# Kernel optimization log

Measured on AMD Instinct MI355X. Metric: run time of the kernel, lower is better.

Reference implementation:

```python
import jax, jax.numpy as jnp
import numpy as np

B, D, H, W, C = 1, 16, 56, 56, 128
NH = 4
WD, WH, WW = 8, 7, 7          # window size (t, h, w)
SD, SH, SW = 4, 3, 3          # shift size
N = WD * WH * WW              # tokens per window = 392
HEAD = C // NH
SCALE = HEAD ** -0.5
HID = 4 * C                   # mlp_ratio = 4
REL_TAB = (2 * WD - 1) * (2 * WH - 1) * (2 * WW - 1)


def _rel_pos_index():
    coords = np.stack(np.meshgrid(np.arange(WD), np.arange(WH), np.arange(WW), indexing='ij'))
    cf = coords.reshape(3, -1)
    rel = (cf[:, :, None] - cf[:, None, :]).transpose(1, 2, 0).astype(np.int64)
    rel[..., 0] += WD - 1; rel[..., 1] += WH - 1; rel[..., 2] += WW - 1
    rel[..., 0] *= (2 * WH - 1) * (2 * WW - 1)
    rel[..., 1] *= (2 * WW - 1)
    return rel.sum(-1)  # (N, N)

REL_IDX = jnp.asarray(_rel_pos_index())


def _win_part_np(x):
    b, d, h, w, c = x.shape
    x = x.reshape(b, d // WD, WD, h // WH, WH, w // WW, WW, c)
    return x.transpose(0, 1, 3, 5, 2, 4, 6, 7).reshape(-1, N, c)


def _attn_mask():
    # shifted-window mask, computed once on host (static)
    img = np.zeros((1, D, H, W, 1))
    cnt = 0
    for ds in (slice(0, -WD), slice(-WD, -SD), slice(-SD, None)):
        for hs in (slice(0, -WH), slice(-WH, -SH), slice(-SH, None)):
            for ws in (slice(0, -WW), slice(-WW, -SW), slice(-SW, None)):
                img[:, ds, hs, ws, :] = cnt
                cnt += 1
    mw = _win_part_np(img).reshape(-1, N)
    am = mw[:, None, :] - mw[:, :, None]
    return np.where(am != 0, -100.0, 0.0).astype(np.float32)  # (nW, N, N)

ATTN_MASK = jnp.asarray(_attn_mask())


def layer_norm(x, w, b, eps=1e-5):
    mu = x.mean(-1, keepdims=True)
    var = ((x - mu) ** 2).mean(-1, keepdims=True)
    return (x - mu) * jax.lax.rsqrt(var + eps) * w + b


def window_partition(x):
    b = x.shape[0]
    x = x.reshape(b, D // WD, WD, H // WH, WH, W // WW, WW, C)
    return x.transpose(0, 1, 3, 5, 2, 4, 6, 7).reshape(-1, N, C)


def window_reverse(win, b):
    x = win.reshape(b, D // WD, H // WH, W // WW, WD, WH, WW, C)
    return x.transpose(0, 1, 4, 2, 5, 3, 6, 7).reshape(b, D, H, W, C)


def setup_inputs() -> dict:
    key = jax.random.key(0)
    ks = jax.random.split(key, 16)
    s = 0.02
    return {
        'x': jax.random.normal(ks[0], (B, D, H, W, C), jnp.float32),
        'norm1_w': jnp.ones((C,), jnp.float32),
        'norm1_b': jnp.zeros((C,), jnp.float32),
        'qkv_w': jax.random.normal(ks[1], (3 * C, C), jnp.float32) * s,
        'qkv_b': jnp.zeros((3 * C,), jnp.float32),
        'rel_pos_table': jax.random.normal(ks[2], (REL_TAB, NH), jnp.float32) * s,
        'proj_w': jax.random.normal(ks[3], (C, C), jnp.float32) * s,
        'proj_b': jnp.zeros((C,), jnp.float32),
        'norm2_w': jnp.ones((C,), jnp.float32),
        'norm2_b': jnp.zeros((C,), jnp.float32),
        'fc1_w': jax.random.normal(ks[4], (HID, C), jnp.float32) * s,
        'fc1_b': jnp.zeros((HID,), jnp.float32),
        'fc2_w': jax.random.normal(ks[5], (C, HID), jnp.float32) * s,
        'fc2_b': jnp.zeros((C,), jnp.float32),
    }


def reference(x, norm1_w, norm1_b, qkv_w, qkv_b, rel_pos_table, proj_w, proj_b,
              norm2_w, norm2_b, fc1_w, fc1_b, fc2_w, fc2_b):
    shortcut = x
    h = layer_norm(x, norm1_w, norm1_b)
    # cyclic shift
    h = jnp.roll(h, shift=(-SD, -SH, -SW), axis=(1, 2, 3))
    win = window_partition(h)                      # (B*nW, N, C)
    Bw = win.shape[0]
    qkv = win @ qkv_w.T + qkv_b                    # (Bw, N, 3C)
    qkv = qkv.reshape(Bw, N, 3, NH, HEAD).transpose(2, 0, 3, 1, 4)
    q, k, v = qkv[0] * SCALE, qkv[1], qkv[2]       # (Bw, NH, N, HEAD)
    bias = rel_pos_table[REL_IDX].transpose(2, 0, 1)  # (NH, N, N)
    A = jnp.einsum('bhnc,bhmc->bhnm', q, k) + bias[None]
    nW = Bw // B
    A = A.reshape(B, nW, NH, N, N) + ATTN_MASK[None, :, None]
    A = jax.nn.softmax(A.reshape(Bw, NH, N, N), axis=-1)
    y = jnp.einsum('bhnm,bhmc->bhnc', A, v).transpose(0, 2, 1, 3).reshape(Bw, N, C)
    y = y @ proj_w.T + proj_b
    h = window_reverse(y, B)
    h = jnp.roll(h, shift=(SD, SH, SW), axis=(1, 2, 3))
    x = shortcut + h
    # Mlp module: internal LayerNorm + residual (see Mlp.forward_fn)
    m = layer_norm(x, norm2_w, norm2_b)
    m = jax.nn.gelu(m @ fc1_w.T + fc1_b, approximate=False)
    m = m @ fc2_w.T + fc2_b
    return x + m
```

## Files before the change

### kernel.cpp

```cpp
#include <hip/hip_runtime.h>
#include <hip/hip_bf16.h>
#include <math.h>


typedef short s16x8 __attribute__((ext_vector_type(8)));
typedef unsigned short u16x8 __attribute__((ext_vector_type(8)));
typedef float fp32x4 __attribute__((ext_vector_type(4)));

#define T_TOT 50176
#define N_TOK 392
#define N_WIN 128

__device__ __forceinline__ unsigned short f2bf(float f) {
    union { float f; unsigned u; } v; v.f = f;
    unsigned r = v.u + 0x7FFFu + ((v.u >> 16) & 1u);
    return (unsigned short)(r >> 16);
}
__device__ __forceinline__ float bf2f(unsigned short u) {
    union { unsigned u; float f; } v; v.u = ((unsigned)u) << 16;
    return v.f;
}

__global__ void cvt_w_k(const float* __restrict__ wq, const float* __restrict__ wp,
                        const float* __restrict__ w1, const float* __restrict__ w2,
                        unsigned short* __restrict__ oq, unsigned short* __restrict__ op,
                        unsigned short* __restrict__ o1, unsigned short* __restrict__ o2)
{
    int i = blockIdx.x * 256 + threadIdx.x;
    if (i < 384 * 128) oq[i] = f2bf(wq[i]);
    if (i < 128 * 128) op[i] = f2bf(wp[i]);
    if (i < 512 * 128) { o1[i] = f2bf(w1[i]); o2[i] = f2bf(w2[i]); }
}

__global__ void bias_tab_k(const float* __restrict__ tab, float* __restrict__ out)
{
    int idx = blockIdx.x * 256 + threadIdx.x;
    if (idx >= 4 * N_TOK * N_TOK) return;
    int h = idx / (N_TOK * N_TOK), r = idx % (N_TOK * N_TOK);
    int i = r / N_TOK, j = r % N_TOK;
    int di = i / 49, hi = (i % 49) / 7, wi = i % 7;
    int dj = j / 49, hj = (j % 49) / 7, wj = j % 7;
    int rel = (di - dj + 7) * 169 + (hi - hj + 6) * 13 + (wi - wj + 6);
    out[idx] = tab[rel * 4 + h];
}

__global__ __launch_bounds__(256) void ln1_part_k(
    const float* __restrict__ x, const float* __restrict__ w,
    const float* __restrict__ b, unsigned short* __restrict__ xw)
{
    const int t = blockIdx.x * 4 + (threadIdx.x >> 6);
    const int lane = threadIdx.x & 63;
    const int win = t / N_TOK, n = t % N_TOK;
    const int wd = win >> 6, wh = (win >> 3) & 7, ww = win & 7;
    const int td = n / 49, rr = n % 49, th = rr / 7, tw = rr % 7;
    const int gd = wd * 8 + td, gh = wh * 7 + th, gw = ww * 7 + tw;
    const int sd = (gd + 4) & 15;
    int sh = gh + 3; if (sh >= 56) sh -= 56;
    int sw = gw + 3; if (sw >= 56) sw -= 56;
    const float* px = x + (((size_t)sd * 56 + sh) * 56 + sw) * 128;
    float v0 = px[lane], v1 = px[lane + 64];
    float s = v0 + v1, s2 = v0 * v0 + v1 * v1;
#pragma unroll
    for (int o = 32; o > 0; o >>= 1) { s += __shfl_xor(s, o); s2 += __shfl_xor(s2, o); }
    float mu = s * (1.f / 128.f);
    float var = s2 * (1.f / 128.f) - mu * mu;
    float rstd = rsqrtf(var + 1e-5f);
    unsigned short* po = xw + (size_t)t * 128;
    po[lane]      = f2bf((v0 - mu) * rstd * w[lane]      + b[lane]);
    po[lane + 64] = f2bf((v1 - mu) * rstd * w[lane + 64] + b[lane + 64]);
}

__global__ __launch_bounds__(256) void ln2_k(
    const float* __restrict__ x1, const float* __restrict__ w,
    const float* __restrict__ b, unsigned short* __restrict__ xn)
{
    const int t = blockIdx.x * 4 + (threadIdx.x >> 6);
    const int lane = threadIdx.x & 63;
    const float* px = x1 + (size_t)t * 128;
    float v0 = px[lane], v1 = px[lane + 64];
    float s = v0 + v1, s2 = v0 * v0 + v1 * v1;
#pragma unroll
    for (int o = 32; o > 0; o >>= 1) { s += __shfl_xor(s, o); s2 += __shfl_xor(s2, o); }
    float mu = s * (1.f / 128.f);
    float var = s2 * (1.f / 128.f) - mu * mu;
    float rstd = rsqrtf(var + 1e-5f);
    unsigned short* po = xn + (size_t)t * 128;
    po[lane]      = f2bf((v0 - mu) * rstd * w[lane]      + b[lane]);
    po[lane + 64] = f2bf((v1 - mu) * rstd * w[lane + 64] + b[lane + 64]);
}

template<int K, int EPI>
__global__ __launch_bounds__(256, 2) void gemm_k(
    const unsigned short* __restrict__ A,
    const unsigned short* __restrict__ Bt,
    const float* __restrict__ bias,
    const float* __restrict__ resid,
    void* __restrict__ outp)
{
    __shared__ __align__(16) unsigned short Asl[128 * 64];
    __shared__ __align__(16) unsigned short Bsl[128 * 64];
    const int bm = blockIdx.x * 128;
    const int bn = blockIdx.y * 128;
    const int tid = threadIdx.x;
    const int lane = tid & 63;
    const int wave = tid >> 6;
    const int wr = wave >> 1, wc = wave & 1;
    const int lr = lane & 15;
    const int lk = (lane >> 4) << 3;

    fp32x4 acc[4][4];
#pragma unroll
    for (int i = 0; i < 4; ++i)
#pragma unroll
        for (int j = 0; j < 4; ++j) acc[i][j] = {0.f, 0.f, 0.f, 0.f};

    for (int ks = 0; ks < K; ks += 64) {
        __syncthreads();
#pragma unroll
        for (int it = 0; it < 4; ++it) {
            int chunk = it * 256 + tid;
            int row = chunk >> 3;
            int kc = (chunk & 7) << 3;
            *(uint4*)&Asl[row * 64 + kc] =
                *(const uint4*)&A[(size_t)(bm + row) * K + ks + kc];
            *(uint4*)&Bsl[row * 64 + kc] =
                *(const uint4*)&Bt[(size_t)(bn + row) * K + ks + kc];
        }
        __syncthreads();
#pragma unroll
        for (int kk = 0; kk < 64; kk += 32) {
            s16x8 af[4], bfr[4];
#pragma unroll
            for (int mb = 0; mb < 4; ++mb)
                af[mb] = *(const s16x8*)&Asl[(wr * 64 + mb * 16 + lr) * 64 + kk + lk];
#pragma unroll
            for (int nb = 0; nb < 4; ++nb)
                bfr[nb] = *(const s16x8*)&Bsl[(wc * 64 + nb * 16 + lr) * 64 + kk + lk];
#pragma unroll
            for (int mb = 0; mb < 4; ++mb)
#pragma unroll
                for (int nb = 0; nb < 4; ++nb)
                    acc[mb][nb] = __builtin_amdgcn_mfma_f32_16x16x32_bf16(
                        af[mb], bfr[nb], acc[mb][nb], 0, 0, 0);
        }
    }

    const int crow = (lane >> 4) << 2;
    const int ccol = lane & 15;
#pragma unroll
    for (int mb = 0; mb < 4; ++mb) {
#pragma unroll
        for (int nb = 0; nb < 4; ++nb) {
#pragma unroll
            for (int r = 0; r < 4; ++r) {
                const int grow = bm + wr * 64 + mb * 16 + crow + r;
                const int gcol = bn + wc * 64 + nb * 16 + ccol;
                float v = acc[mb][nb][r] + bias[gcol];
                if (EPI == 0) {
                    if (gcol < 128) v *= 0.17677669529663687f;
                    ((unsigned short*)outp)[(size_t)grow * 384 + gcol] = f2bf(v);
                } else if (EPI == 1) {
                    int w  = grow / N_TOK, n = grow % N_TOK;
                    int wd = w >> 6, wh = (w >> 3) & 7, ww = w & 7;
                    int td = n / 49, rr = n % 49, th = rr / 7, tw = rr % 7;
                    int gd = wd * 8 + td, gh = wh * 7 + th, gw = ww * 7 + tw;
                    int sd = (gd + 4) & 15;
                    int sh = gh + 3; if (sh >= 56) sh -= 56;
                    int sw = gw + 3; if (sw >= 56) sw -= 56;
                    size_t oi = (((size_t)sd * 56 + sh) * 56 + sw) * 128 + gcol;
                    ((float*)outp)[oi] = v + resid[oi];
                } else if (EPI == 2) {
                    v = 0.5f * v * (1.f + erff(v * 0.70710678118654752f));
                    ((unsigned short*)outp)[(size_t)grow * 512 + gcol] = f2bf(v);
                } else {
                    size_t oi = (size_t)grow * 128 + gcol;
                    ((float*)outp)[oi] = v + resid[oi];
                }
            }
        }
    }
}

#define KSTR 40
#define VSTR 424
#define PTS  40

__global__ __launch_bounds__(256, 2) void attn_k(
    const unsigned short* __restrict__ qkv,
    const float* __restrict__ btab,
    unsigned short* __restrict__ y)
{
    __shared__ __align__(16) unsigned short Ksh[416 * KSTR];
    __shared__ __align__(16) unsigned short Vt[32 * VSTR];
    __shared__ __align__(16) unsigned short Pt[4][16 * PTS];
    __shared__ __align__(4) unsigned char rid_sh[416];

    const int blk = blockIdx.x;
    const int wI = blk >> 2, h = blk & 3;
    const int tid = threadIdx.x;
    const int wave = tid >> 6, lane = tid & 63;
    const int lr = lane & 15, g = lane >> 4, lk = g << 3;
    const unsigned short* base = qkv + (size_t)wI * N_TOK * 384;

    const int wd = wI >> 6, wh = (wI >> 3) & 7, ww = wI & 7;
    const bool boundary = (wd == 1) | (wh == 7) | (ww == 7);

    for (int idx = tid; idx < 392 * 4; idx += 256) {
        int j = idx >> 2, c0 = (idx & 3) << 3;
        *(uint4*)&Ksh[j * KSTR + c0] =
            *(const uint4*)&base[(size_t)j * 384 + 128 + h * 32 + c0];
    }
    for (int idx = tid; idx < 24 * 4; idx += 256) {
        int j = 392 + (idx >> 2), c0 = (idx & 3) << 3;
        u16x8 z = {};
        *(u16x8*)&Ksh[j * KSTR + c0] = z;
    }
    for (int idx = tid; idx < 32 * 49; idx += 256) {
        int c = idx & 31, j0 = (idx >> 5) << 3;
        const unsigned short* vp = base + 256 + h * 32 + c;
        u16x8 tmp;
#pragma unroll
        for (int i = 0; i < 8; ++i) tmp[i] = vp[(size_t)(j0 + i) * 384];
        *(u16x8*)&Vt[c * VSTR + j0] = tmp;
    }
    for (int idx = tid; idx < 32 * 3; idx += 256) {
        int c = idx & 31, j0 = 392 + ((idx >> 5) << 3);
        u16x8 z = {};
        *(u16x8*)&Vt[c * VSTR + j0] = z;
    }
    for (int n = tid; n < 416; n += 256) {
        int nn = (n < 392) ? n : 391;
        int td = nn / 49, rr = nn % 49, th = rr / 7, tw = rr % 7;
        int gd = wd * 8 + td, gh = wh * 7 + th, gw = ww * 7 + tw;
        int r = ((gd < 8) ? 0 : ((gd < 12) ? 9 : 18)) +
                ((gh < 49) ? 0 : ((gh < 53) ? 3 : 6)) +
                ((gw < 49) ? 0 : ((gw < 53) ? 1 : 2));
        rid_sh[n] = (unsigned char)r;
    }
    __syncthreads();

    const float* bb = btab + (size_t)h * N_TOK * N_TOK;
    unsigned short* pw = &Pt[wave][0];
    const int j0 = g << 2;

    for (int rt = wave; rt < 25; rt += 4) {
        const int irow = rt * 16 + lr;
        const int ic = (irow < 392) ? irow : 391;
        s16x8 bq = *(const s16x8*)&base[(size_t)ic * 384 + h * 32 + lk];
        fp32x4 acc[25];
#pragma unroll
        for (int ct = 0; ct < 25; ++ct) {
            s16x8 ak = *(const s16x8*)&Ksh[(ct * 16 + lr) * KSTR + lk];
            fp32x4 z = {0.f, 0.f, 0.f, 0.f};
            acc[ct] = __builtin_amdgcn_mfma_f32_16x16x32_bf16(ak, bq, z, 0, 0, 0);
        }
        const int ri = rid_sh[ic];
        float mx = -1e30f;
#pragma unroll
        for (int ct = 0; ct < 24; ++ct) {
            float4 bv = *(const float4*)&bb[(size_t)ic * N_TOK + ct * 16 + j0];
            unsigned rj4 = *(const unsigned*)&rid_sh[ct * 16 + j0];
            const float bs[4] = {bv.x, bv.y, bv.z, bv.w};
#pragma unroll
            for (int r = 0; r < 4; ++r) {
                float s = acc[ct][r] + bs[r];
                int rj = (rj4 >> (8 * r)) & 255;
                if (boundary && rj != ri) s -= 100.f;
                acc[ct][r] = s;
                mx = fmaxf(mx, s);
            }
        }
        {
            float4 bv = {0.f, 0.f, 0.f, 0.f};
            unsigned rj4 = 0;
            if (g < 2) {
                bv = *(const float4*)&bb[(size_t)ic * N_TOK + 384 + j0];
                rj4 = *(const unsigned*)&rid_sh[384 + j0];
            }
            const float bs[4] = {bv.x, bv.y, bv.z, bv.w};
#pragma unroll
            for (int r = 0; r < 4; ++r) {
                float s = -1e30f;
                if (g < 2) {
                    s = acc[24][r] + bs[r];
                    int rj = (rj4 >> (8 * r)) & 255;
                    if (boundary && rj != ri) s -= 100.f;
                }
                acc[24][r] = s;
                mx = fmaxf(mx, s);
            }
        }
        mx = fmaxf(mx, __shfl_xor(mx, 16));
        mx = fmaxf(mx, __shfl_xor(mx, 32));
        float sum = 0.f;
#pragma unroll
        for (int ct = 0; ct < 25; ++ct)
#pragma unroll
            for (int r = 0; r < 4; ++r) {
                float p = __expf(acc[ct][r] - mx);
                acc[ct][r] = p;
                sum += p;
            }
        sum += __shfl_xor(sum, 16);
        sum += __shfl_xor(sum, 32);
        const float rs = 1.f / sum;
        fp32x4 o0 = {0.f, 0.f, 0.f, 0.f}, o1 = {0.f, 0.f, 0.f, 0.f};
#pragma unroll
        for (int ks = 0; ks < 13; ++ks) {
            unsigned w0, w1, w2 = 0, w3 = 0;
            asm("v_cvt_pk_bf16_f32 %0, %1, %2"
                : "=v"(w0) : "v"(acc[2 * ks][0]), "v"(acc[2 * ks][1]));
            asm("v_cvt_pk_bf16_f32 %0, %1, %2"
                : "=v"(w1) : "v"(acc[2 * ks][2]), "v"(acc[2 * ks][3]));
            if (ks < 12) {
                asm("v_cvt_pk_bf16_f32 %0, %1, %2"
                    : "=v"(w2) : "v"(acc[2 * ks + 1][0]), "v"(acc[2 * ks + 1][1]));
                asm("v_cvt_pk_bf16_f32 %0, %1, %2"
                    : "=v"(w3) : "v"(acc[2 * ks + 1][2]), "v"(acc[2 * ks + 1][3]));
            }
            *(unsigned*)&pw[lr * PTS + j0]          = w0;
            *(unsigned*)&pw[lr * PTS + j0 + 2]      = w1;
            *(unsigned*)&pw[lr * PTS + 16 + j0]     = w2;
            *(unsigned*)&pw[lr * PTS + 16 + j0 + 2] = w3;
            s16x8 ap  = *(const s16x8*)&pw[lr * PTS + lk];
            s16x8 bv0 = *(const s16x8*)&Vt[lr * VSTR + ks * 32 + lk];
            s16x8 bv1 = *(const s16x8*)&Vt[(16 + lr) * VSTR + ks * 32 + lk];
            o0 = __builtin_amdgcn_mfma_f32_16x16x32_bf16(ap, bv0, o0, 0, 0, 0);
            o1 = __builtin_amdgcn_mfma_f32_16x16x32_bf16(ap, bv1, o1, 0, 0, 0);
        }
#pragma unroll
        for (int r = 0; r < 4; ++r) {
            const float rsr = __shfl(rs, (g << 2) + r);
            const int row = rt * 16 + (g << 2) + r;
            if (row < 392) {
                size_t ob = ((size_t)wI * N_TOK + row) * 128 + h * 32;
                y[ob + lr]      = f2bf(o0[r] * rsr);
                y[ob + 16 + lr] = f2bf(o1[r] * rsr);
            }
        }
    }
}

extern "C" void kernel_launch(void* const* d_in, const int* in_sizes, int n_in,
                              void* d_out, int out_size, void* d_ws, size_t ws_size,
                              hipStream_t stream)
{
    const float* x      = (const float*)d_in[0];
    const float* n1w    = (const float*)d_in[1];
    const float* n1b    = (const float*)d_in[2];
    const float* qkv_w  = (const float*)d_in[3];
    const float* qkv_b  = (const float*)d_in[4];
    const float* rpt    = (const float*)d_in[5];
    const float* proj_w = (const float*)d_in[6];
    const float* proj_b = (const float*)d_in[7];
    const float* n2w    = (const float*)d_in[8];
    const float* n2b    = (const float*)d_in[9];
    const float* fc1_w  = (const float*)d_in[10];
    const float* fc1_b  = (const float*)d_in[11];
    const float* fc2_w  = (const float*)d_in[12];
    const float* fc2_b  = (const float*)d_in[13];

    char* ws = (char*)d_ws;
    unsigned short* xw  = (unsigned short*)(ws);
    unsigned short* qkv = (unsigned short*)(ws + 12845056);
    unsigned short* y   = (unsigned short*)(ws + 51380224);
    float*          x1  = (float*)         (ws + 64225280);
    unsigned short* xn  = (unsigned short*)(ws + 89915392);
    unsigned short* hid = (unsigned short*)(ws + 102760448);
    unsigned short* wq  = (unsigned short*)(ws + 154140672);
    unsigned short* wp  = (unsigned short*)(ws + 154238976);
    unsigned short* w1  = (unsigned short*)(ws + 154271744);
    unsigned short* w2  = (unsigned short*)(ws + 154402816);
    float*          bt  = (float*)         (ws + 154533888);

    hipLaunchKernelGGL(cvt_w_k, dim3(256), dim3(256), 0, stream,
                       qkv_w, proj_w, fc1_w, fc2_w, wq, wp, w1, w2);
    hipLaunchKernelGGL(bias_tab_k, dim3((4 * N_TOK * N_TOK + 255) / 256), dim3(256),
                       0, stream, rpt, bt);
    hipLaunchKernelGGL(ln1_part_k, dim3(T_TOT / 4), dim3(256), 0, stream,
                       x, n1w, n1b, xw);
    hipLaunchKernelGGL((gemm_k<128, 0>), dim3(392, 3), dim3(256), 0, stream,
                       xw, wq, qkv_b, (const float*)nullptr, (void*)qkv);
    hipLaunchKernelGGL(attn_k, dim3(512), dim3(256), 0, stream, qkv, bt, y);
    hipLaunchKernelGGL((gemm_k<128, 1>), dim3(392, 1), dim3(256), 0, stream,
                       y, wp, proj_b, x, (void*)x1);
    hipLaunchKernelGGL(ln2_k, dim3(T_TOT / 4), dim3(256), 0, stream,
                       x1, n2w, n2b, xn);
    hipLaunchKernelGGL((gemm_k<128, 2>), dim3(392, 4), dim3(256), 0, stream,
                       xn, w1, fc1_b, (const float*)nullptr, (void*)hid);
    hipLaunchKernelGGL((gemm_k<512, 3>), dim3(392, 1), dim3(256), 0, stream,
                       hid, w2, fc2_b, x1, d_out);
}
```

Measured before the change: 257.2 us.

## Fuse LayerNorm2 into proj GEMM epilogue and precombine shift mask with bias

The proj GEMM epilogue now stages its tile in shared memory, adds the residual, and computes LayerNorm2 row by row. It writes both x1 and the normalized bf16 input for fc1, which removes the separate ln2 kernel and its re-read of x1. The relative-position bias table is also expanded into 8 mask variants per head with the -100 shift mask already applied, so the attention kernel does a plain float4 add instead of building region IDs and comparing them. The cost is a bias-table build eight times larger each call, which aliases into the hid buffer, and a larger shared-memory footprint in the EPI==1 GEMM.

```diff
diff --git a/kernel.cpp b/kernel.cpp
--- a/kernel.cpp
+++ b/kernel.cpp
@@ -10,6 +10,7 @@
 #define T_TOT 50176
 #define N_TOK 392
 #define N_WIN 128
+#define NN2 153664
 
 __device__ __forceinline__ unsigned short f2bf(float f) {
     union { float f; unsigned u; } v; v.f = f;
@@ -35,13 +36,22 @@
 __global__ void bias_tab_k(const float* __restrict__ tab, float* __restrict__ out)
 {
     int idx = blockIdx.x * 256 + threadIdx.x;
-    if (idx >= 4 * N_TOK * N_TOK) return;
-    int h = idx / (N_TOK * N_TOK), r = idx % (N_TOK * N_TOK);
+    if (idx >= 32 * NN2) return;
+    int ht = idx / NN2, r = idx % NN2;
+    int h = ht >> 3, type = ht & 7;
     int i = r / N_TOK, j = r % N_TOK;
     int di = i / 49, hi = (i % 49) / 7, wi = i % 7;
     int dj = j / 49, hj = (j % 49) / 7, wj = j % 7;
     int rel = (di - dj + 7) * 169 + (hi - hj + 6) * 13 + (wi - wj + 6);
-    out[idx] = tab[rel * 4 + h];
+    float v = tab[rel * 4 + h];
+    int ri = ((type & 4) ? (di < 4 ? 9 : 18) : 0) +
+             ((type & 2) ? (hi < 4 ? 3 : 6) : 0) +
+             ((type & 1) ? (wi < 4 ? 1 : 2) : 0);
+    int rj = ((type & 4) ? (dj < 4 ? 9 : 18) : 0) +
+             ((type & 2) ? (hj < 4 ? 3 : 6) : 0) +
+             ((type & 1) ? (wj < 4 ? 1 : 2) : 0);
+    if (ri != rj) v -= 100.f;
+    out[idx] = v;
 }
 
 __global__ __launch_bounds__(256) void ln1_part_k(
@@ -70,35 +80,21 @@
     po[lane + 64] = f2bf((v1 - mu) * rstd * w[lane + 64] + b[lane + 64]);
 }
 
-__global__ __launch_bounds__(256) void ln2_k(
-    const float* __restrict__ x1, const float* __restrict__ w,
-    const float* __restrict__ b, unsigned short* __restrict__ xn)
-{
-    const int t = blockIdx.x * 4 + (threadIdx.x >> 6);
-    const int lane = threadIdx.x & 63;
-    const float* px = x1 + (size_t)t * 128;
-    float v0 = px[lane], v1 = px[lane + 64];
-    float s = v0 + v1, s2 = v0 * v0 + v1 * v1;
-#pragma unroll
-    for (int o = 32; o > 0; o >>= 1) { s += __shfl_xor(s, o); s2 += __shfl_xor(s2, o); }
-    float mu = s * (1.f / 128.f);
-    float var = s2 * (1.f / 128.f) - mu * mu;
-    float rstd = rsqrtf(var + 1e-5f);
-    unsigned short* po = xn + (size_t)t * 128;
-    po[lane]      = f2bf((v0 - mu) * rstd * w[lane]      + b[lane]);
-    po[lane + 64] = f2bf((v1 - mu) * rstd * w[lane + 64] + b[lane + 64]);
-}
-
 template<int K, int EPI>
 __global__ __launch_bounds__(256, 2) void gemm_k(
     const unsigned short* __restrict__ A,
     const unsigned short* __restrict__ Bt,
     const float* __restrict__ bias,
     const float* __restrict__ resid,
-    void* __restrict__ outp)
-{
-    __shared__ __align__(16) unsigned short Asl[128 * 64];
-    __shared__ __align__(16) unsigned short Bsl[128 * 64];
+    const float* __restrict__ lnw,
+    const float* __restrict__ lnb,
+    void* __restrict__ outp,
+    void* __restrict__ outp2)
+{
+    constexpr int SMB = (EPI == 1) ? (128 * 132 * 4) : (2 * 128 * 64 * 2);
+    __shared__ __align__(16) char smem[SMB];
+    unsigned short* Asl = (unsigned short*)smem;
+    unsigned short* Bsl = Asl + 128 * 64;
     const int bm = blockIdx.x * 128;
     const int bn = blockIdx.y * 128;
     const int tid = threadIdx.x;
@@ -147,6 +143,51 @@
 
     const int crow = (lane >> 4) << 2;
     const int ccol = lane & 15;
+
+    if (EPI == 1) {
+        float* xs = (float*)smem;
+        __syncthreads();
+#pragma unroll
+        for (int mb = 0; mb < 4; ++mb)
+#pragma unroll
+            for (int nb = 0; nb < 4; ++nb)
+#pragma unroll
+                for (int r = 0; r < 4; ++r) {
+                    int row = wr * 64 + mb * 16 + crow + r;
+                    int col = wc * 64 + nb * 16 + ccol;
+                    xs[row * 132 + col] = acc[mb][nb][r] + bias[col];
+                }
+        __syncthreads();
+        const float wA = lnw[lane], wB = lnw[lane + 64];
+        const float bA = lnb[lane], bB = lnb[lane + 64];
+        float* x1o = (float*)outp;
+        unsigned short* xno = (unsigned short*)outp2;
+        for (int row = wave; row < 128; row += 4) {
+            const int grow = bm + row;
+            const int w = grow / N_TOK, n = grow % N_TOK;
+            const int wd = w >> 6, wh = (w >> 3) & 7, ww = w & 7;
+            const int td = n / 49, rr = n % 49, th = rr / 7, tw = rr % 7;
+            const int gd = wd * 8 + td, gh = wh * 7 + th, gw = ww * 7 + tw;
+            const int sd = (gd + 4) & 15;
+            int sh = gh + 3; if (sh >= 56) sh -= 56;
+            int sw = gw + 3; if (sw >= 56) sw -= 56;
+            const size_t tok = ((size_t)sd * 56 + sh) * 56 + sw;
+            float w0 = xs[row * 132 + lane]      + resid[tok * 128 + lane];
+            float w1 = xs[row * 132 + 64 + lane] + resid[tok * 128 + 64 + lane];
+            float s = w0 + w1, s2 = w0 * w0 + w1 * w1;
+#pragma unroll
+            for (int o = 32; o > 0; o >>= 1) { s += __shfl_xor(s, o); s2 += __shfl_xor(s2, o); }
+            float mu = s * (1.f / 128.f);
+            float var = s2 * (1.f / 128.f) - mu * mu;
+            float rstd = rsqrtf(var + 1e-5f);
+            x1o[tok * 128 + lane]      = w0;
+            x1o[tok * 128 + 64 + lane] = w1;
+            xno[tok * 128 + lane]      = f2bf((w0 - mu) * rstd * wA + bA);
+            xno[tok * 128 + 64 + lane] = f2bf((w1 - mu) * rstd * wB + bB);
+        }
+        return;
+    }
+
 #pragma unroll
     for (int mb = 0; mb < 4; ++mb) {
 #pragma unroll
@@ -159,16 +200,6 @@
                 if (EPI == 0) {
                     if (gcol < 128) v *= 0.17677669529663687f;
                     ((unsigned short*)outp)[(size_t)grow * 384 + gcol] = f2bf(v);
-                } else if (EPI == 1) {
-                    int w  = grow / N_TOK, n = grow % N_TOK;
-                    int wd = w >> 6, wh = (w >> 3) & 7, ww = w & 7;
-                    int td = n / 49, rr = n % 49, th = rr / 7, tw = rr % 7;
-                    int gd = wd * 8 + td, gh = wh * 7 + th, gw = ww * 7 + tw;
-                    int sd = (gd + 4) & 15;
-                    int sh = gh + 3; if (sh >= 56) sh -= 56;
-                    int sw = gw + 3; if (sw >= 56) sw -= 56;
-                    size_t oi = (((size_t)sd * 56 + sh) * 56 + sw) * 128 + gcol;
-                    ((float*)outp)[oi] = v + resid[oi];
                 } else if (EPI == 2) {
                     v = 0.5f * v * (1.f + erff(v * 0.70710678118654752f));
                     ((unsigned short*)outp)[(size_t)grow * 512 + gcol] = f2bf(v);
@@ -187,13 +218,12 @@
 
 __global__ __launch_bounds__(256, 2) void attn_k(
     const unsigned short* __restrict__ qkv,
-    const float* __restrict__ btab,
+    const float* __restrict__ cbias,
     unsigned short* __restrict__ y)
 {
     __shared__ __align__(16) unsigned short Ksh[416 * KSTR];
     __shared__ __align__(16) unsigned short Vt[32 * VSTR];
     __shared__ __align__(16) unsigned short Pt[4][16 * PTS];
-    __shared__ __align__(4) unsigned char rid_sh[416];
 
     const int blk = blockIdx.x;
     const int wI = blk >> 2, h = blk & 3;
@@ -203,7 +233,7 @@
     const unsigned short* base = qkv + (size_t)wI * N_TOK * 384;
 
     const int wd = wI >> 6, wh = (wI >> 3) & 7, ww = wI & 7;
-    const bool boundary = (wd == 1) | (wh == 7) | (ww == 7);
+    const int type = ((wd == 1) ? 4 : 0) | ((wh == 7) ? 2 : 0) | ((ww == 7) ? 1 : 0);
 
     for (int idx = tid; idx < 392 * 4; idx += 256) {
         int j = idx >> 2, c0 = (idx & 3) << 3;
@@ -216,30 +246,21 @@
         *(u16x8*)&Ksh[j * KSTR + c0] = z;
     }
     for (int idx = tid; idx < 32 * 49; idx += 256) {
-        int c = idx & 31, j0 = (idx >> 5) << 3;
+        int c = idx & 31, j0v = (idx >> 5) << 3;
         const unsigned short* vp = base + 256 + h * 32 + c;
         u16x8 tmp;
 #pragma unroll
-        for (int i = 0; i < 8; ++i) tmp[i] = vp[(size_t)(j0 + i) * 384];
-        *(u16x8*)&Vt[c * VSTR + j0] = tmp;
+        for (int i = 0; i < 8; ++i) tmp[i] = vp[(size_t)(j0v + i) * 384];
+        *(u16x8*)&Vt[c * VSTR + j0v] = tmp;
     }
     for (int idx = tid; idx < 32 * 3; idx += 256) {
-        int c = idx & 31, j0 = 392 + ((idx >> 5) << 3);
+        int c = idx & 31, j0v = 392 + ((idx >> 5) << 3);
         u16x8 z = {};
-        *(u16x8*)&Vt[c * VSTR + j0] = z;
-    }
-    for (int n = tid; n < 416; n += 256) {
-        int nn = (n < 392) ? n : 391;
-        int td = nn / 49, rr = nn % 49, th = rr / 7, tw = rr % 7;
-        int gd = wd * 8 + td, gh = wh * 7 + th, gw = ww * 7 + tw;
-        int r = ((gd < 8) ? 0 : ((gd < 12) ? 9 : 18)) +
-                ((gh < 49) ? 0 : ((gh < 53) ? 3 : 6)) +
-                ((gw < 49) ? 0 : ((gw < 53) ? 1 : 2));
-        rid_sh[n] = (unsigned char)r;
+        *(u16x8*)&Vt[c * VSTR + j0v] = z;
     }
     __syncthreads();
 
-    const float* bb = btab + (size_t)h * N_TOK * N_TOK;
+    const float* cbb = cbias + (size_t)(h * 8 + type) * NN2;
     unsigned short* pw = &Pt[wave][0];
     const int j0 = g << 2;
 
@@ -254,40 +275,25 @@
             fp32x4 z = {0.f, 0.f, 0.f, 0.f};
             acc[ct] = __builtin_amdgcn_mfma_f32_16x16x32_bf16(ak, bq, z, 0, 0, 0);
         }
-        const int ri = rid_sh[ic];
+        const float* cbr = cbb + (size_t)ic * N_TOK;
         float mx = -1e30f;
 #pragma unroll
         for (int ct = 0; ct < 24; ++ct) {
-            float4 bv = *(const float4*)&bb[(size_t)ic * N_TOK + ct * 16 + j0];
-            unsigned rj4 = *(const unsigned*)&rid_sh[ct * 16 + j0];
-            const float bs[4] = {bv.x, bv.y, bv.z, bv.w};
-#pragma unroll
-            for (int r = 0; r < 4; ++r) {
-                float s = acc[ct][r] + bs[r];
-                int rj = (rj4 >> (8 * r)) & 255;
-                if (boundary && rj != ri) s -= 100.f;
-                acc[ct][r] = s;
-                mx = fmaxf(mx, s);
-            }
+            float4 bv = *(const float4*)&cbr[ct * 16 + j0];
+            acc[ct][0] += bv.x; acc[ct][1] += bv.y;
+            acc[ct][2] += bv.z; acc[ct][3] += bv.w;
+            mx = fmaxf(mx, fmaxf(fmaxf(acc[ct][0], acc[ct][1]),
+                                 fmaxf(acc[ct][2], acc[ct][3])));
         }
         {
-            float4 bv = {0.f, 0.f, 0.f, 0.f};
-            unsigned rj4 = 0;
             if (g < 2) {
-                bv = *(const float4*)&bb[(size_t)ic * N_TOK + 384 + j0];
-                rj4 = *(const unsigned*)&rid_sh[384 + j0];
-            }
-            const float bs[4] = {bv.x, bv.y, bv.z, bv.w};
-#pragma unroll
-            for (int r = 0; r < 4; ++r) {
-                float s = -1e30f;
-                if (g < 2) {
-                    s = acc[24][r] + bs[r];
-                    int rj = (rj4 >> (8 * r)) & 255;
-                    if (boundary && rj != ri) s -= 100.f;
-                }
-                acc[24][r] = s;
-                mx = fmaxf(mx, s);
+                float4 bv = *(const float4*)&cbr[384 + j0];
+                acc[24][0] += bv.x; acc[24][1] += bv.y;
+                acc[24][2] += bv.z; acc[24][3] += bv.w;
+                mx = fmaxf(mx, fmaxf(fmaxf(acc[24][0], acc[24][1]),
+                                     fmaxf(acc[24][2], acc[24][3])));
+            } else {
+                acc[24][0] = acc[24][1] = acc[24][2] = acc[24][3] = -1e30f;
             }
         }
         mx = fmaxf(mx, __shfl_xor(mx, 16));
@@ -367,27 +373,31 @@
     float*          x1  = (float*)         (ws + 64225280);
     unsigned short* xn  = (unsigned short*)(ws + 89915392);
     unsigned short* hid = (unsigned short*)(ws + 102760448);
+    float*          cb  = (float*)         (ws + 102760448);
     unsigned short* wq  = (unsigned short*)(ws + 154140672);
     unsigned short* wp  = (unsigned short*)(ws + 154238976);
     unsigned short* w1  = (unsigned short*)(ws + 154271744);
     unsigned short* w2  = (unsigned short*)(ws + 154402816);
-    float*          bt  = (float*)         (ws + 154533888);
 
     hipLaunchKernelGGL(cvt_w_k, dim3(256), dim3(256), 0, stream,
                        qkv_w, proj_w, fc1_w, fc2_w, wq, wp, w1, w2);
-    hipLaunchKernelGGL(bias_tab_k, dim3((4 * N_TOK * N_TOK + 255) / 256), dim3(256),
-                       0, stream, rpt, bt);
+    hipLaunchKernelGGL(bias_tab_k, dim3((32 * NN2 + 255) / 256), dim3(256),
+                       0, stream, rpt, cb);
     hipLaunchKernelGGL(ln1_part_k, dim3(T_TOT / 4), dim3(256), 0, stream,
                        x, n1w, n1b, xw);
     hipLaunchKernelGGL((gemm_k<128, 0>), dim3(392, 3), dim3(256), 0, stream,
-                       xw, wq, qkv_b, (const float*)nullptr, (void*)qkv);
-    hipLaunchKernelGGL(attn_k, dim3(512), dim3(256), 0, stream, qkv, bt, y);
+                       xw, wq, qkv_b, (const float*)nullptr,
+                       (const float*)nullptr, (const float*)nullptr,
+                       (void*)qkv, (void*)nullptr);
+    hipLaunchKernelGGL(attn_k, dim3(512), dim3(256), 0, stream, qkv, cb, y);
     hipLaunchKernelGGL((gemm_k<128, 1>), dim3(392, 1), dim3(256), 0, stream,
-                       y, wp, proj_b, x, (void*)x1);
-    hipLaunchKernelGGL(ln2_k, dim3(T_TOT / 4), dim3(256), 0, stream,
-                       x1, n2w, n2b, xn);
+                       y, wp, proj_b, x, n2w, n2b, (void*)x1, (void*)xn);
     hipLaunchKernelGGL((gemm_k<128, 2>), dim3(392, 4), dim3(256), 0, stream,
-                       xn, w1, fc1_b, (const float*)nullptr, (void*)hid);
+                       xn, w1, fc1_b, (const float*)nullptr,
+                       (const float*)nullptr, (const float*)nullptr,
+                       (void*)hid, (void*)nullptr);
     hipLaunchKernelGGL((gemm_k<512, 3>), dim3(392, 1), dim3(256), 0, stream,
-                       hid, w2, fc2_b, x1, d_out);
-}
+                       hid, w2, fc2_b, x1,
+                       (const float*)nullptr, (const float*)nullptr,
+                       d_out, (void*)nullptr);
+}
```

New measurement: 263.1 us. 1.02x slower.
